# Kernel tuning notes

Hardware: AMD Instinct MI355X
Metric: run time of the kernel (lower is better)

Reference implementation:

```python
import jax, jax.numpy as jnp
import numpy as np

N = 100000   # nodes
E = 3200000  # edges (avg degree 32)
K = 3        # num_stacks
L = 4        # num_layers (ARMA iterations)
H = 16       # hidden channels
C = 1        # num_classes
BN_EPS = 1e-5


def setup_inputs() -> dict:
    key = jax.random.key(0)
    ks = jax.random.split(key, 16)
    s = 0.1  # weight scale
    return {
        "x": jax.random.normal(ks[0], (N, 1), dtype=jnp.float32),
        "edge_index": jax.random.randint(ks[1], (2, E), 0, N, dtype=jnp.int64),
        "edge_attr": jax.random.uniform(ks[2], (E,), dtype=jnp.float32),
        "batch": jnp.zeros((N,), dtype=jnp.int64),
        # ARMAConv 1: 1 -> 16, shared weights
        "w1_init": s * jax.random.normal(ks[3], (K, 1, H), dtype=jnp.float32),
        "w1": s * jax.random.normal(ks[4], (K, H, H), dtype=jnp.float32),
        "w1_root": s * jax.random.normal(ks[5], (K, 1, H), dtype=jnp.float32),
        "b1": s * jax.random.normal(ks[6], (K, 1, H), dtype=jnp.float32),
        "bn1_g": jnp.ones((H,), dtype=jnp.float32),
        "bn1_b": jnp.zeros((H,), dtype=jnp.float32),
        # ARMAConv 2: 16 -> 1, shared weights, act=None
        "w2_init": s * jax.random.normal(ks[7], (K, H, C), dtype=jnp.float32),
        "w2": s * jax.random.normal(ks[8], (K, C, C), dtype=jnp.float32),
        "w2_root": s * jax.random.normal(ks[9], (K, H, C), dtype=jnp.float32),
        "b2": s * jax.random.normal(ks[10], (K, 1, C), dtype=jnp.float32),
    }


def _arma_conv(x, row, col, norm, w_init, w, w_root, b, n_layers, use_relu):
    """PyG ARMAConv with shared_weights=True, eval-mode dropout (identity).
    x: [N,Fin]; returns mean over K stacks: [N,Fout]."""
    n = x.shape[0]
    root = jnp.einsum('nf,kfo->kno', x, w_root)      # [K,N,Fout]
    out = jnp.einsum('nf,kfo->kno', x, w_init)       # [K,N,Fout]
    for t in range(n_layers):
        if t > 0:
            out = jnp.einsum('kno,kop->knp', out, w)
        # message: gather at source, scale by norm; aggregate (scatter-add) at target
        m = (out[:, row, :] * norm[None, :, None]).transpose(1, 0, 2)  # [E,K,F]
        out = jax.ops.segment_sum(m, col, num_segments=n).transpose(1, 0, 2)
        out = out + root + b
        if use_relu:
            out = jax.nn.relu(out)
    return out.mean(axis=0)


def reference(x, edge_index, edge_attr, batch, w1_init, w1, w1_root, b1,
              bn1_g, bn1_b, w2_init, w2, w2_root, b2):
    row, col = edge_index[0], edge_index[1]
    n = x.shape[0]
    # gcn_norm without self-loops: D^{-1/2} A D^{-1/2}
    deg = jax.ops.segment_sum(edge_attr, col, num_segments=n)
    dinv = jnp.where(deg > 0, jax.lax.rsqrt(jnp.maximum(deg, 1e-12)), 0.0)
    norm = dinv[row] * edge_attr * dinv[col]

    h = _arma_conv(x, row, col, norm, w1_init, w1, w1_root, b1, L, True)
    # BatchNorm1d (batch statistics) + ReLU; dropout is identity in eval
    mu = h.mean(axis=0)
    var = h.var(axis=0)
    h = (h - mu) * jax.lax.rsqrt(var + BN_EPS) * bn1_g + bn1_b
    h = jax.nn.relu(h)

    h = _arma_conv(h, row, col, norm, w2_init, w2, w2_root, b2, L, False)
    return jax.nn.sigmoid(h)
```

## Files before the change

### kernel.cpp

```cpp
#include <hip/hip_runtime.h>
#include <math.h>

#define N_NODES 100000
#define N_EDGES 3200000
#define KH 48
#define FDIM 64
#define NH 16
#define BN_EPS 1e-5f
#define NBUCK 196
#define BSHIFT 9
#define BMASK 511
#define EPB 16384
#define NBLK1 196
#define CAP 18432
#define FIX 16777216.0f

typedef unsigned long long u64;
typedef unsigned int u32;
typedef unsigned short u16;

__device__ __forceinline__ u16 f2bf(float f) {
  u32 b = __float_as_uint(f);
  b += 0x7FFFu + ((b >> 16) & 1u);
  return (u16)(b >> 16);
}
__device__ __forceinline__ float bf2f(u32 s) {
  return __uint_as_float(s << 16);
}

__global__ __launch_bounds__(1024) void bucket_scatter_kernel(
    const int* __restrict__ row, const int* __restrict__ col,
    const float* __restrict__ ea, u32* __restrict__ gcur,
    int2* __restrict__ bucketed) {
  __shared__ u32 bins[NBUCK];
  __shared__ u32 base[NBUCK];
  __shared__ u16 rnk[EPB];
  for (int t = threadIdx.x; t < NBUCK; t += 1024) bins[t] = 0;
  __syncthreads();
  int eb = blockIdx.x * EPB;
  for (int it = 0; it < EPB / 1024; ++it) {
    int i = it * 1024 + threadIdx.x;
    int e = eb + i;
    if (e < N_EDGES) rnk[i] = (u16)atomicAdd(&bins[col[e] >> BSHIFT], 1u);
  }
  __syncthreads();
  for (int t = threadIdx.x; t < NBUCK; t += 1024) {
    u32 c = bins[t];
    if (c) base[t] = (u32)t * CAP + atomicAdd(&gcur[t * 8], c);
  }
  __syncthreads();
  for (int it = 0; it < EPB / 1024; ++it) {
    int i = it * 1024 + threadIdx.x;
    int e = eb + i;
    if (e < N_EDGES) {
      int c = col[e];
      int bkt = c >> BSHIFT, cl = c & BMASK;
      u32 pos = base[bkt] + (u32)rnk[i];
      bucketed[pos] = make_int2((cl << 17) | row[e], __float_as_int(ea[e]));
    }
  }
}

__global__ __launch_bounds__(1024) void node_offs_kernel(
    const int2* __restrict__ bucketed, const u32* __restrict__ gcur,
    const float* __restrict__ x,
    int* __restrict__ offs, float* __restrict__ dinv, u16* __restrict__ zx) {
  __shared__ u32 cnt[512];
  __shared__ u32 degf[512];
  __shared__ u32 red[256];
  __shared__ u32 shmeta[2];
  int t = threadIdx.x;
  int b = blockIdx.x;
  if (t < 512) { cnt[t] = 0; degf[t] = 0; }
  if (t < 256) red[t] = (t < b) ? gcur[t * 8] : 0;
  __syncthreads();
  for (int d = 128; d; d >>= 1) {
    if (t < d) red[t] += red[t + d];
    __syncthreads();
  }
  if (t == 0) { shmeta[0] = red[0]; shmeta[1] = gcur[b * 8]; }
  __syncthreads();
  u32 bst = shmeta[0], fill = shmeta[1];
  u32 s_pad = (u32)b * CAP;
  for (u32 i = t; i < fill; i += 1024) {
    int2 v = bucketed[s_pad + i];
    int cl = (v.x >> 17) & BMASK;
    atomicAdd(&cnt[cl], 1u);
    atomicAdd(&degf[cl], (u32)(__int_as_float(v.y) * FIX));
  }
  __syncthreads();
  u32 v0 = (t < 512) ? cnt[t] : 0;
  for (int d = 1; d < 512; d <<= 1) {
    u32 u = (t < 512 && t >= d) ? cnt[t - d] : 0;
    __syncthreads();
    if (t < 512) cnt[t] += u;
    __syncthreads();
  }
  int n = b * 512 + t;
  if (t < 512 && n < N_NODES) {
    offs[n] = (int)(bst + cnt[t] - v0);
    float dg = (float)degf[t] * (1.0f / FIX);
    float dv = dg > 0.f ? rsqrtf(fmaxf(dg, 1e-12f)) : 0.f;
    dinv[n] = dv;
    zx[n] = f2bf(x[n] * dv);
  }
  if (b == 0 && t == 0) offs[N_NODES] = N_EDGES;
}

__global__ __launch_bounds__(1024) void csr_fill_kernel(
    const int2* __restrict__ bucketed, const u32* __restrict__ gcur,
    const int* __restrict__ offs, u32* __restrict__ csr) {
  __shared__ u32 cur[512];
  __shared__ u32 shfill;
  int t = threadIdx.x;
  int b = blockIdx.x;
  int n = b * 512 + t;
  if (t < 512) cur[t] = (n < N_NODES) ? (u32)offs[n] : 0;
  if (t == 0) shfill = gcur[b * 8];
  __syncthreads();
  u32 fill = shfill;
  u32 s_pad = (u32)b * CAP;
  for (u32 i = t; i < fill; i += 1024) {
    int2 v = bucketed[s_pad + i];
    int cl = (v.x >> 17) & BMASK;
    u32 r = (u32)(v.x & 0x1FFFF);
    u16 w = f2bf(__int_as_float(v.y));
    u32 pos = atomicAdd(&cur[cl], 1u);
    csr[pos] = (r << 15) | (u32)w;
  }
}

__global__ __launch_bounds__(256) void sprop_mid_kernel(
    const u32* __restrict__ csr, const int* __restrict__ offs,
    const u16* __restrict__ zx, const float* __restrict__ dinv,
    const float* __restrict__ x,
    const float* __restrict__ w1i, const float* __restrict__ w1r,
    const float* __restrict__ b1, const float* __restrict__ w1,
    u16* __restrict__ tout) {
  int t = blockIdx.x * 256 + threadIdx.x;
  int n = t >> 4, c = t & 15;
  float a = 0.f;
  int s = offs[n], e = offs[n + 1];
  for (int i = s + c; i < e; i += 16) {
    u32 ee = csr[i];
    a += bf2f(ee & 0x7FFFu) * bf2f((u32)zx[ee >> 15]);
  }
#pragma unroll
  for (int o = 8; o; o >>= 1) a += __shfl_xor(a, o, 64);
  float dn = dinv[n];
  float sn = a * dn;
  float xn = x[n];
  int base = (threadIdx.x & 63) & 48;
#pragma unroll
  for (int k = 0; k < 3; ++k) {
    float u = fmaxf(sn * w1i[k * 16 + c] + xn * w1r[k * 16 + c] + b1[k * 16 + c], 0.f);
    float tf = 0.f;
#pragma unroll
    for (int f = 0; f < 16; ++f) tf += __shfl(u, base + f, 64) * w1[k * 256 + f * 16 + c];
    tout[(size_t)n * FDIM + k * 16 + c] = f2bf(tf * dn);
  }
}

__global__ __launch_bounds__(256) void conv1_prop_kernel(
    const u16* __restrict__ tin, u16* __restrict__ tout, float* __restrict__ hbuf,
    const u32* __restrict__ csr, const int* __restrict__ offs,
    const float* __restrict__ dinv, const float* __restrict__ x,
    const float* __restrict__ w1r, const float* __restrict__ b1,
    const float* __restrict__ w1, int do_t) {
  int lane = threadIdx.x & 63;
  int wid = (blockIdx.x * blockDim.x + threadIdx.x) >> 6;
  int nw = (gridDim.x * blockDim.x) >> 6;
  int c = lane;
  bool act = c < KH;
  float rb = act ? w1r[c] : 0.f;
  float bb = act ? b1[c] : 0.f;
  float wreg[16];
  if (do_t) {
    int k = c >> 4, o = c & 15;
    if (act) {
#pragma unroll
      for (int f = 0; f < 16; ++f) wreg[f] = w1[k * 256 + f * 16 + o];
    } else {
#pragma unroll
      for (int f = 0; f < 16; ++f) wreg[f] = 0.f;
    }
  }
  for (int n = wid; n < N_NODES; n += nw) {
    int nu = __builtin_amdgcn_readfirstlane(n);
    int s = offs[nu], e = offs[nu + 1];
    float acc = 0.f;
    int i = s;
    for (; i + 16 <= e; i += 16) {
      u32 e0 = __builtin_nontemporal_load(&csr[i]);
      u32 e1 = __builtin_nontemporal_load(&csr[i + 1]);
      u32 e2 = __builtin_nontemporal_load(&csr[i + 2]);
      u32 e3 = __builtin_nontemporal_load(&csr[i + 3]);
      u32 e4 = __builtin_nontemporal_load(&csr[i + 4]);
      u32 e5 = __builtin_nontemporal_load(&csr[i + 5]);
      u32 e6 = __builtin_nontemporal_load(&csr[i + 6]);
      u32 e7 = __builtin_nontemporal_load(&csr[i + 7]);
      u32 e8 = __builtin_nontemporal_load(&csr[i + 8]);
      u32 e9 = __builtin_nontemporal_load(&csr[i + 9]);
      u32 ea0 = __builtin_nontemporal_load(&csr[i + 10]);
      u32 eb0 = __builtin_nontemporal_load(&csr[i + 11]);
      u32 ec0 = __builtin_nontemporal_load(&csr[i + 12]);
      u32 ed0 = __builtin_nontemporal_load(&csr[i + 13]);
      u32 ee0 = __builtin_nontemporal_load(&csr[i + 14]);
      u32 ef0 = __builtin_nontemporal_load(&csr[i + 15]);
      float v0 = 0.f, v1 = 0.f, v2 = 0.f, v3 = 0.f;
      float v4 = 0.f, v5 = 0.f, v6 = 0.f, v7 = 0.f;
      float v8 = 0.f, v9 = 0.f, va = 0.f, vb = 0.f;
      float vc = 0.f, vd = 0.f, ve = 0.f, vf = 0.f;
      if (act) {
        v0 = bf2f((u32)tin[(e0 >> 15) * FDIM + c]);
        v1 = bf2f((u32)tin[(e1 >> 15) * FDIM + c]);
        v2 = bf2f((u32)tin[(e2 >> 15) * FDIM + c]);
        v3 = bf2f((u32)tin[(e3 >> 15) * FDIM + c]);
        v4 = bf2f((u32)tin[(e4 >> 15) * FDIM + c]);
        v5 = bf2f((u32)tin[(e5 >> 15) * FDIM + c]);
        v6 = bf2f((u32)tin[(e6 >> 15) * FDIM + c]);
        v7 = bf2f((u32)tin[(e7 >> 15) * FDIM + c]);
        v8 = bf2f((u32)tin[(e8 >> 15) * FDIM + c]);
        v9 = bf2f((u32)tin[(e9 >> 15) * FDIM + c]);
        va = bf2f((u32)tin[(ea0 >> 15) * FDIM + c]);
        vb = bf2f((u32)tin[(eb0 >> 15) * FDIM + c]);
        vc = bf2f((u32)tin[(ec0 >> 15) * FDIM + c]);
        vd = bf2f((u32)tin[(ed0 >> 15) * FDIM + c]);
        ve = bf2f((u32)tin[(ee0 >> 15) * FDIM + c]);
        vf = bf2f((u32)tin[(ef0 >> 15) * FDIM + c]);
      }
      acc += bf2f(e0 & 0x7FFFu) * v0 + bf2f(e1 & 0x7FFFu) * v1 +
             bf2f(e2 & 0x7FFFu) * v2 + bf2f(e3 & 0x7FFFu) * v3 +
             bf2f(e4 & 0x7FFFu) * v4 + bf2f(e5 & 0x7FFFu) * v5 +
             bf2f(e6 & 0x7FFFu) * v6 + bf2f(e7 & 0x7FFFu) * v7 +
             bf2f(e8 & 0x7FFFu) * v8 + bf2f(e9 & 0x7FFFu) * v9 +
             bf2f(ea0 & 0x7FFFu) * va + bf2f(eb0 & 0x7FFFu) * vb +
             bf2f(ec0 & 0x7FFFu) * vc + bf2f(ed0 & 0x7FFFu) * vd +
             bf2f(ee0 & 0x7FFFu) * ve + bf2f(ef0 & 0x7FFFu) * vf;
    }
    for (; i + 8 <= e; i += 8) {
      u32 e0 = __builtin_nontemporal_load(&csr[i]);
      u32 e1 = __builtin_nontemporal_load(&csr[i + 1]);
      u32 e2 = __builtin_nontemporal_load(&csr[i + 2]);
      u32 e3 = __builtin_nontemporal_load(&csr[i + 3]);
      u32 e4 = __builtin_nontemporal_load(&csr[i + 4]);
      u32 e5 = __builtin_nontemporal_load(&csr[i + 5]);
      u32 e6 = __builtin_nontemporal_load(&csr[i + 6]);
      u32 e7 = __builtin_nontemporal_load(&csr[i + 7]);
      float v0 = 0.f, v1 = 0.f, v2 = 0.f, v3 = 0.f;
      float v4 = 0.f, v5 = 0.f, v6 = 0.f, v7 = 0.f;
      if (act) {
        v0 = bf2f((u32)tin[(e0 >> 15) * FDIM + c]);
        v1 = bf2f((u32)tin[(e1 >> 15) * FDIM + c]);
        v2 = bf2f((u32)tin[(e2 >> 15) * FDIM + c]);
        v3 = bf2f((u32)tin[(e3 >> 15) * FDIM + c]);
        v4 = bf2f((u32)tin[(e4 >> 15) * FDIM + c]);
        v5 = bf2f((u32)tin[(e5 >> 15) * FDIM + c]);
        v6 = bf2f((u32)tin[(e6 >> 15) * FDIM + c]);
        v7 = bf2f((u32)tin[(e7 >> 15) * FDIM + c]);
      }
      acc += bf2f(e0 & 0x7FFFu) * v0 + bf2f(e1 & 0x7FFFu) * v1 +
             bf2f(e2 & 0x7FFFu) * v2 + bf2f(e3 & 0x7FFFu) * v3 +
             bf2f(e4 & 0x7FFFu) * v4 + bf2f(e5 & 0x7FFFu) * v5 +
             bf2f(e6 & 0x7FFFu) * v6 + bf2f(e7 & 0x7FFFu) * v7;
    }
    for (; i + 4 <= e; i += 4) {
      u32 e0 = __builtin_nontemporal_load(&csr[i]);
      u32 e1 = __builtin_nontemporal_load(&csr[i + 1]);
      u32 e2 = __builtin_nontemporal_load(&csr[i + 2]);
      u32 e3 = __builtin_nontemporal_load(&csr[i + 3]);
      float v0 = 0.f, v1 = 0.f, v2 = 0.f, v3 = 0.f;
      if (act) {
        v0 = bf2f((u32)tin[(e0 >> 15) * FDIM + c]);
        v1 = bf2f((u32)tin[(e1 >> 15) * FDIM + c]);
        v2 = bf2f((u32)tin[(e2 >> 15) * FDIM + c]);
        v3 = bf2f((u32)tin[(e3 >> 15) * FDIM + c]);
      }
      acc += bf2f(e0 & 0x7FFFu) * v0 + bf2f(e1 & 0x7FFFu) * v1 +
             bf2f(e2 & 0x7FFFu) * v2 + bf2f(e3 & 0x7FFFu) * v3;
    }
    for (; i < e; ++i) {
      u32 ee = __builtin_nontemporal_load(&csr[i]);
      if (act) acc += bf2f(ee & 0x7FFFu) * bf2f((u32)tin[(ee >> 15) * FDIM + c]);
    }
    float dn = dinv[nu];
    float u = fmaxf(acc * dn + x[nu] * rb + bb, 0.f);
    if (do_t) {
      float tf = 0.f;
      int base = c & 48;
#pragma unroll
      for (int f = 0; f < 16; ++f) tf += __shfl(u, base + f, 64) * wreg[f];
      if (act) tout[(size_t)nu * FDIM + c] = f2bf(tf * dn);
    } else {
      float m1v = __shfl(u, lane + 16, 64);
      float m2v = __shfl(u, lane + 32, 64);
      if (lane < NH) hbuf[(size_t)nu * NH + lane] = (u + m1v + m2v) * (1.f / 3.f);
    }
  }
}

__global__ __launch_bounds__(256) void bn_stats_kernel(
    const float* __restrict__ h, double* __restrict__ stats) {
  __shared__ float ssum[NH], ssq[NH];
  int tid = threadIdx.x;
  if (tid < NH) { ssum[tid] = 0.f; ssq[tid] = 0.f; }
  __syncthreads();
  int n = blockIdx.x * blockDim.x + tid;
  bool valid = n < N_NODES;
  const float4* p = (const float4*)(h + (size_t)(valid ? n : 0) * NH);
  float hv[NH];
#pragma unroll
  for (int q = 0; q < 4; ++q) {
    float4 v = valid ? p[q] : make_float4(0.f, 0.f, 0.f, 0.f);
    hv[q * 4 + 0] = v.x; hv[q * 4 + 1] = v.y; hv[q * 4 + 2] = v.z; hv[q * 4 + 3] = v.w;
  }
#pragma unroll
  for (int f = 0; f < NH; ++f) {
    float s = hv[f], q = hv[f] * hv[f];
    for (int o = 32; o; o >>= 1) { s += __shfl_xor(s, o, 64); q += __shfl_xor(q, o, 64); }
    if ((tid & 63) == 0) { atomicAdd(&ssum[f], s); atomicAdd(&ssq[f], q); }
  }
  __syncthreads();
  if (tid < NH) {
    atomicAdd(&stats[tid], (double)ssum[tid]);
    atomicAdd(&stats[NH + tid], (double)ssq[tid]);
  }
}

__global__ __launch_bounds__(64) void bn_final_kernel(
    const double* __restrict__ stats, const float* __restrict__ g,
    const float* __restrict__ b, float* __restrict__ sc, float* __restrict__ sh) {
  int f = threadIdx.x;
  if (f < NH) {
    double mu = stats[f] / (double)N_NODES;
    double var = stats[NH + f] / (double)N_NODES - mu * mu;
    float scale = g[f] * (float)(1.0 / sqrt(var + (double)BN_EPS));
    sc[f] = scale;
    sh[f] = b[f] - (float)mu * scale;
  }
}

__global__ __launch_bounds__(256) void conv2_init_kernel(
    const float* __restrict__ h, const float* __restrict__ sc, const float* __restrict__ sh,
    const float* __restrict__ dinv,
    const float* __restrict__ w2i, const float* __restrict__ w2r, const float* __restrict__ b2,
    float* __restrict__ P, float* __restrict__ R) {
  int n = blockIdx.x * blockDim.x + threadIdx.x;
  if (n >= N_NODES) return;
  float u[NH];
#pragma unroll
  for (int f = 0; f < NH; ++f) u[f] = fmaxf(h[(size_t)n * NH + f] * sc[f] + sh[f], 0.f);
  float dn = dinv[n];
#pragma unroll
  for (int k = 0; k < 3; ++k) {
    float r = b2[k], o = 0.f;
#pragma unroll
    for (int f = 0; f < NH; ++f) {
      r += u[f] * w2r[k * NH + f];
      o += u[f] * w2i[k * NH + f];
    }
    R[n * 4 + k] = r;
    P[n * 4 + k] = o * dn;
  }
  R[n * 4 + 3] = 0.f;
  P[n * 4 + 3] = 0.f;
}

__global__ __launch_bounds__(256) void conv2_prop_kernel(
    const float* __restrict__ in4, float* __restrict__ out4, float* __restrict__ y,
    const u32* __restrict__ csr, const int* __restrict__ offs,
    const float* __restrict__ dinv,
    const float* __restrict__ R, const float* __restrict__ w2,
    int scale_w2, int final_out) {
  int t = blockIdx.x * 256 + threadIdx.x;
  int n = t >> 4, sub = t & 15;
  float m0 = 1.f, m1 = 1.f, m2 = 1.f;
  if (scale_w2) { m0 = w2[0]; m1 = w2[1]; m2 = w2[2]; }
  int s = offs[n], e = offs[n + 1];
  float a0 = 0.f, a1 = 0.f, a2 = 0.f;
  for (int i = s + sub; i < e; i += 16) {
    u32 ee = csr[i];
    float w = bf2f(ee & 0x7FFFu);
    const float4 v = *(const float4*)(in4 + (size_t)(ee >> 15) * 4);
    a0 += w * v.x;
    a1 += w * v.y;
    a2 += w * v.z;
  }
#pragma unroll
  for (int o = 8; o; o >>= 1) {
    a0 += __shfl_xor(a0, o, 64);
    a1 += __shfl_xor(a1, o, 64);
    a2 += __shfl_xor(a2, o, 64);
  }
  if (sub == 0) {
    float dn = dinv[n];
    a0 = a0 * dn * m0 + R[n * 4 + 0];
    a1 = a1 * dn * m1 + R[n * 4 + 1];
    a2 = a2 * dn * m2 + R[n * 4 + 2];
    if (final_out) {
      float sm = (a0 + a1 + a2) * (1.f / 3.f);
      y[n] = 1.f / (1.f + expf(-sm));
    } else {
      out4[n * 4 + 0] = a0 * dn;
      out4[n * 4 + 1] = a1 * dn;
      out4[n * 4 + 2] = a2 * dn;
      out4[n * 4 + 3] = 0.f;
    }
  }
}

extern "C" void kernel_launch(void* const* d_in, const int* in_sizes, int n_in,
                              void* d_out, int out_size, void* d_ws, size_t ws_size,
                              hipStream_t stream) {
  const float* x   = (const float*)d_in[0];
  const int*   ei  = (const int*)d_in[1];
  const float* ea  = (const float*)d_in[2];
  const float* w1i = (const float*)d_in[4];
  const float* w1  = (const float*)d_in[5];
  const float* w1r = (const float*)d_in[6];
  const float* b1  = (const float*)d_in[7];
  const float* bng = (const float*)d_in[8];
  const float* bnb = (const float*)d_in[9];
  const float* w2i = (const float*)d_in[10];
  const float* w2  = (const float*)d_in[11];
  const float* w2r = (const float*)d_in[12];
  const float* b2  = (const float*)d_in[13];
  float* y = (float*)d_out;

  const int* row = ei;
  const int* col = ei + N_EDGES;

  char* ws = (char*)d_ws;
  size_t off = 0;
  auto alloc = [&](size_t bytes) -> char* {
    char* p = ws + off;
    off += (bytes + 255) & ~(size_t)255;
    return p;
  };
  u32*    gcur   = (u32*)alloc((size_t)NBUCK * 8 * 4);
  int*    offs   = (int*)alloc((size_t)(N_NODES + 1) * 4);
  float*  dinv   = (float*)alloc((size_t)N_NODES * 4);
  u16*    zx     = (u16*)alloc((size_t)N_NODES * 2);
  double* stats  = (double*)alloc(32 * 8);
  float*  bnsc   = (float*)alloc(16 * 4);
  float*  bnsh   = (float*)alloc(16 * 4);
  int2*   bucketed = (int2*)alloc((size_t)NBUCK * CAP * 8);
  u32*    csr    = (u32*)alloc((size_t)N_EDGES * 4);
  u16*    tA     = (u16*)alloc((size_t)N_NODES * FDIM * 2);
  u16*    tB     = (u16*)alloc((size_t)N_NODES * FDIM * 2);
  float*  hbuf   = (float*)alloc((size_t)N_NODES * NH * 4);
  float*  P2     = (float*)alloc((size_t)N_NODES * 4 * 4);
  float*  Q2     = (float*)alloc((size_t)N_NODES * 4 * 4);
  float*  R2     = (float*)alloc((size_t)N_NODES * 4 * 4);
  (void)ws_size; (void)in_sizes; (void)n_in; (void)out_size;

  hipMemsetAsync(gcur, 0, (size_t)NBUCK * 8 * 4, stream);
  hipMemsetAsync(stats, 0, 32 * 8, stream);

  bucket_scatter_kernel<<<NBLK1, 1024, 0, stream>>>(row, col, ea, gcur, bucketed);
  node_offs_kernel<<<NBUCK, 1024, 0, stream>>>(bucketed, gcur, x, offs, dinv, zx);
  csr_fill_kernel<<<NBUCK, 1024, 0, stream>>>(bucketed, gcur, offs, csr);

  const int NPB = 6250;
  sprop_mid_kernel<<<NPB, 256, 0, stream>>>(csr, offs, zx, dinv, x, w1i, w1r, b1, w1, tA);
  conv1_prop_kernel<<<6250, 256, 0, stream>>>(tA, tB, nullptr, csr, offs, dinv, x, w1r, b1, w1, 1);
  conv1_prop_kernel<<<6250, 256, 0, stream>>>(tB, tA, nullptr, csr, offs, dinv, x, w1r, b1, w1, 1);
  conv1_prop_kernel<<<6250, 256, 0, stream>>>(tA, nullptr, hbuf, csr, offs, dinv, x, w1r, b1, w1, 0);

  bn_stats_kernel<<<(N_NODES + 255) / 256, 256, 0, stream>>>(hbuf, stats);
  bn_final_kernel<<<1, 64, 0, stream>>>(stats, bng, bnb, bnsc, bnsh);
  conv2_init_kernel<<<(N_NODES + 255) / 256, 256, 0, stream>>>(
      hbuf, bnsc, bnsh, dinv, w2i, w2r, b2, P2, R2);

  conv2_prop_kernel<<<NPB, 256, 0, stream>>>(P2, Q2, nullptr, csr, offs, dinv, R2, w2, 0, 0);
  conv2_prop_kernel<<<NPB, 256, 0, stream>>>(Q2, P2, nullptr, csr, offs, dinv, R2, w2, 1, 0);
  conv2_prop_kernel<<<NPB, 256, 0, stream>>>(P2, Q2, nullptr, csr, offs, dinv, R2, w2, 1, 0);
  conv2_prop_kernel<<<NPB, 256, 0, stream>>>(Q2, P2, y, csr, offs, dinv, R2, w2, 1, 1);
}
```

Baseline: 472.2 us.

## Split conv1 propagation per stack with stack-major layout and sub-wave edge parallelism

Stores the conv1 features stack-major (K x N x 16 bf16) instead of interleaved 64-wide rows. Each propagation pass now launches one grid slice per stack. Within a wave, the four 16-lane groups each take a different edge, using vector loads of the CSR plus shuffle reductions, so no lanes sit idle as before. The stack mean moves into the BN stats and conv2 init kernels, which now read three hbuf planes. The trade-off is three times as many CSR reads and more gather requests with narrower 32-byte rows.

```diff
diff --git a/kernel.cpp b/kernel.cpp
--- a/kernel.cpp
+++ b/kernel.cpp
@@ -3,9 +3,8 @@
 
 #define N_NODES 100000
 #define N_EDGES 3200000
-#define KH 48
-#define FDIM 64
 #define NH 16
+#define SST (N_NODES * NH)
 #define BN_EPS 1e-5f
 #define NBUCK 196
 #define BSHIFT 9
@@ -14,10 +13,14 @@
 #define NBLK1 196
 #define CAP 18432
 #define FIX 16777216.0f
+#define NBLKS 6250
+#define NWAVES 25000
 
 typedef unsigned long long u64;
 typedef unsigned int u32;
 typedef unsigned short u16;
+typedef __attribute__((ext_vector_type(4))) unsigned int u32x4;
+typedef __attribute__((ext_vector_type(2))) unsigned int u32x2;
 
 __device__ __forceinline__ u16 f2bf(float f) {
   u32 b = __float_as_uint(f);
@@ -157,144 +160,78 @@
     float tf = 0.f;
 #pragma unroll
     for (int f = 0; f < 16; ++f) tf += __shfl(u, base + f, 64) * w1[k * 256 + f * 16 + c];
-    tout[(size_t)n * FDIM + k * 16 + c] = f2bf(tf * dn);
+    tout[(size_t)k * SST + (size_t)n * NH + c] = f2bf(tf * dn);
   }
 }
 
 __global__ __launch_bounds__(256) void conv1_prop_kernel(
-    const u16* __restrict__ tin, u16* __restrict__ tout, float* __restrict__ hbuf,
+    const u16* __restrict__ tin, u16* __restrict__ tout, float* __restrict__ hbuf3,
     const u32* __restrict__ csr, const int* __restrict__ offs,
     const float* __restrict__ dinv, const float* __restrict__ x,
     const float* __restrict__ w1r, const float* __restrict__ b1,
     const float* __restrict__ w1, int do_t) {
+  int k = blockIdx.x / NBLKS;
+  int bid = blockIdx.x - k * NBLKS;
   int lane = threadIdx.x & 63;
-  int wid = (blockIdx.x * blockDim.x + threadIdx.x) >> 6;
-  int nw = (gridDim.x * blockDim.x) >> 6;
-  int c = lane;
-  bool act = c < KH;
-  float rb = act ? w1r[c] : 0.f;
-  float bb = act ? b1[c] : 0.f;
-  float wreg[16];
+  int sub = lane >> 4;
+  int c = lane & 15;
+  int wid = ((bid << 8) + (int)threadIdx.x) >> 6;
+  const u16* __restrict__ tk = tin + (size_t)k * SST;
+  float rb = w1r[k * NH + c];
+  float bb = b1[k * NH + c];
+  int srcbase = sub * 20;
+  float wreg[4];
   if (do_t) {
-    int k = c >> 4, o = c & 15;
-    if (act) {
-#pragma unroll
-      for (int f = 0; f < 16; ++f) wreg[f] = w1[k * 256 + f * 16 + o];
-    } else {
-#pragma unroll
-      for (int f = 0; f < 16; ++f) wreg[f] = 0.f;
-    }
-  }
-  for (int n = wid; n < N_NODES; n += nw) {
+#pragma unroll
+    for (int j = 0; j < 4; ++j) wreg[j] = w1[k * 256 + (sub * 4 + j) * NH + c];
+  }
+  for (int n = wid; n < N_NODES; n += NWAVES) {
     int nu = __builtin_amdgcn_readfirstlane(n);
     int s = offs[nu], e = offs[nu + 1];
+    float dn = dinv[nu];
+    float xn = x[nu];
     float acc = 0.f;
     int i = s;
+    int la = (4 - (i & 3)) & 3;
+    if (la > e - i) la = e - i;
+    if (sub < la) {
+      u32 ee = __builtin_nontemporal_load(csr + i + sub);
+      acc += bf2f(ee & 0x7FFFu) * bf2f((u32)tk[(ee >> 15) * NH + c]);
+    }
+    i += la;
     for (; i + 16 <= e; i += 16) {
-      u32 e0 = __builtin_nontemporal_load(&csr[i]);
-      u32 e1 = __builtin_nontemporal_load(&csr[i + 1]);
-      u32 e2 = __builtin_nontemporal_load(&csr[i + 2]);
-      u32 e3 = __builtin_nontemporal_load(&csr[i + 3]);
-      u32 e4 = __builtin_nontemporal_load(&csr[i + 4]);
-      u32 e5 = __builtin_nontemporal_load(&csr[i + 5]);
-      u32 e6 = __builtin_nontemporal_load(&csr[i + 6]);
-      u32 e7 = __builtin_nontemporal_load(&csr[i + 7]);
-      u32 e8 = __builtin_nontemporal_load(&csr[i + 8]);
-      u32 e9 = __builtin_nontemporal_load(&csr[i + 9]);
-      u32 ea0 = __builtin_nontemporal_load(&csr[i + 10]);
-      u32 eb0 = __builtin_nontemporal_load(&csr[i + 11]);
-      u32 ec0 = __builtin_nontemporal_load(&csr[i + 12]);
-      u32 ed0 = __builtin_nontemporal_load(&csr[i + 13]);
-      u32 ee0 = __builtin_nontemporal_load(&csr[i + 14]);
-      u32 ef0 = __builtin_nontemporal_load(&csr[i + 15]);
-      float v0 = 0.f, v1 = 0.f, v2 = 0.f, v3 = 0.f;
-      float v4 = 0.f, v5 = 0.f, v6 = 0.f, v7 = 0.f;
-      float v8 = 0.f, v9 = 0.f, va = 0.f, vb = 0.f;
-      float vc = 0.f, vd = 0.f, ve = 0.f, vf = 0.f;
-      if (act) {
-        v0 = bf2f((u32)tin[(e0 >> 15) * FDIM + c]);
-        v1 = bf2f((u32)tin[(e1 >> 15) * FDIM + c]);
-        v2 = bf2f((u32)tin[(e2 >> 15) * FDIM + c]);
-        v3 = bf2f((u32)tin[(e3 >> 15) * FDIM + c]);
-        v4 = bf2f((u32)tin[(e4 >> 15) * FDIM + c]);
-        v5 = bf2f((u32)tin[(e5 >> 15) * FDIM + c]);
-        v6 = bf2f((u32)tin[(e6 >> 15) * FDIM + c]);
-        v7 = bf2f((u32)tin[(e7 >> 15) * FDIM + c]);
-        v8 = bf2f((u32)tin[(e8 >> 15) * FDIM + c]);
-        v9 = bf2f((u32)tin[(e9 >> 15) * FDIM + c]);
-        va = bf2f((u32)tin[(ea0 >> 15) * FDIM + c]);
-        vb = bf2f((u32)tin[(eb0 >> 15) * FDIM + c]);
-        vc = bf2f((u32)tin[(ec0 >> 15) * FDIM + c]);
-        vd = bf2f((u32)tin[(ed0 >> 15) * FDIM + c]);
-        ve = bf2f((u32)tin[(ee0 >> 15) * FDIM + c]);
-        vf = bf2f((u32)tin[(ef0 >> 15) * FDIM + c]);
-      }
-      acc += bf2f(e0 & 0x7FFFu) * v0 + bf2f(e1 & 0x7FFFu) * v1 +
-             bf2f(e2 & 0x7FFFu) * v2 + bf2f(e3 & 0x7FFFu) * v3 +
-             bf2f(e4 & 0x7FFFu) * v4 + bf2f(e5 & 0x7FFFu) * v5 +
-             bf2f(e6 & 0x7FFFu) * v6 + bf2f(e7 & 0x7FFFu) * v7 +
-             bf2f(e8 & 0x7FFFu) * v8 + bf2f(e9 & 0x7FFFu) * v9 +
-             bf2f(ea0 & 0x7FFFu) * va + bf2f(eb0 & 0x7FFFu) * vb +
-             bf2f(ec0 & 0x7FFFu) * vc + bf2f(ed0 & 0x7FFFu) * vd +
-             bf2f(ee0 & 0x7FFFu) * ve + bf2f(ef0 & 0x7FFFu) * vf;
+      u32x4 q = __builtin_nontemporal_load((const u32x4*)(csr + i) + sub);
+      acc += bf2f(q.x & 0x7FFFu) * bf2f((u32)tk[(q.x >> 15) * NH + c]);
+      acc += bf2f(q.y & 0x7FFFu) * bf2f((u32)tk[(q.y >> 15) * NH + c]);
+      acc += bf2f(q.z & 0x7FFFu) * bf2f((u32)tk[(q.z >> 15) * NH + c]);
+      acc += bf2f(q.w & 0x7FFFu) * bf2f((u32)tk[(q.w >> 15) * NH + c]);
     }
     for (; i + 8 <= e; i += 8) {
-      u32 e0 = __builtin_nontemporal_load(&csr[i]);
-      u32 e1 = __builtin_nontemporal_load(&csr[i + 1]);
-      u32 e2 = __builtin_nontemporal_load(&csr[i + 2]);
-      u32 e3 = __builtin_nontemporal_load(&csr[i + 3]);
-      u32 e4 = __builtin_nontemporal_load(&csr[i + 4]);
-      u32 e5 = __builtin_nontemporal_load(&csr[i + 5]);
-      u32 e6 = __builtin_nontemporal_load(&csr[i + 6]);
-      u32 e7 = __builtin_nontemporal_load(&csr[i + 7]);
-      float v0 = 0.f, v1 = 0.f, v2 = 0.f, v3 = 0.f;
-      float v4 = 0.f, v5 = 0.f, v6 = 0.f, v7 = 0.f;
-      if (act) {
-        v0 = bf2f((u32)tin[(e0 >> 15) * FDIM + c]);
-        v1 = bf2f((u32)tin[(e1 >> 15) * FDIM + c]);
-        v2 = bf2f((u32)tin[(e2 >> 15) * FDIM + c]);
-        v3 = bf2f((u32)tin[(e3 >> 15) * FDIM + c]);
-        v4 = bf2f((u32)tin[(e4 >> 15) * FDIM + c]);
-        v5 = bf2f((u32)tin[(e5 >> 15) * FDIM + c]);
-        v6 = bf2f((u32)tin[(e6 >> 15) * FDIM + c]);
-        v7 = bf2f((u32)tin[(e7 >> 15) * FDIM + c]);
-      }
-      acc += bf2f(e0 & 0x7FFFu) * v0 + bf2f(e1 & 0x7FFFu) * v1 +
-             bf2f(e2 & 0x7FFFu) * v2 + bf2f(e3 & 0x7FFFu) * v3 +
-             bf2f(e4 & 0x7FFFu) * v4 + bf2f(e5 & 0x7FFFu) * v5 +
-             bf2f(e6 & 0x7FFFu) * v6 + bf2f(e7 & 0x7FFFu) * v7;
+      u32x2 q = __builtin_nontemporal_load((const u32x2*)(csr + i) + sub);
+      acc += bf2f(q.x & 0x7FFFu) * bf2f((u32)tk[(q.x >> 15) * NH + c]);
+      acc += bf2f(q.y & 0x7FFFu) * bf2f((u32)tk[(q.y >> 15) * NH + c]);
     }
     for (; i + 4 <= e; i += 4) {
-      u32 e0 = __builtin_nontemporal_load(&csr[i]);
-      u32 e1 = __builtin_nontemporal_load(&csr[i + 1]);
-      u32 e2 = __builtin_nontemporal_load(&csr[i + 2]);
-      u32 e3 = __builtin_nontemporal_load(&csr[i + 3]);
-      float v0 = 0.f, v1 = 0.f, v2 = 0.f, v3 = 0.f;
-      if (act) {
-        v0 = bf2f((u32)tin[(e0 >> 15) * FDIM + c]);
-        v1 = bf2f((u32)tin[(e1 >> 15) * FDIM + c]);
-        v2 = bf2f((u32)tin[(e2 >> 15) * FDIM + c]);
-        v3 = bf2f((u32)tin[(e3 >> 15) * FDIM + c]);
-      }
-      acc += bf2f(e0 & 0x7FFFu) * v0 + bf2f(e1 & 0x7FFFu) * v1 +
-             bf2f(e2 & 0x7FFFu) * v2 + bf2f(e3 & 0x7FFFu) * v3;
-    }
-    for (; i < e; ++i) {
-      u32 ee = __builtin_nontemporal_load(&csr[i]);
-      if (act) acc += bf2f(ee & 0x7FFFu) * bf2f((u32)tin[(ee >> 15) * FDIM + c]);
-    }
-    float dn = dinv[nu];
-    float u = fmaxf(acc * dn + x[nu] * rb + bb, 0.f);
+      u32 ee = __builtin_nontemporal_load(csr + i + sub);
+      acc += bf2f(ee & 0x7FFFu) * bf2f((u32)tk[(ee >> 15) * NH + c]);
+    }
+    int rem = e - i;
+    if (sub < rem) {
+      u32 ee = __builtin_nontemporal_load(csr + i + sub);
+      acc += bf2f(ee & 0x7FFFu) * bf2f((u32)tk[(ee >> 15) * NH + c]);
+    }
+    acc += __shfl_xor(acc, 16, 64);
+    acc += __shfl_xor(acc, 32, 64);
+    float u = fmaxf(acc * dn + xn * rb + bb, 0.f);
     if (do_t) {
       float tf = 0.f;
-      int base = c & 48;
-#pragma unroll
-      for (int f = 0; f < 16; ++f) tf += __shfl(u, base + f, 64) * wreg[f];
-      if (act) tout[(size_t)nu * FDIM + c] = f2bf(tf * dn);
+#pragma unroll
+      for (int j = 0; j < 4; ++j) tf += __shfl(u, srcbase + j, 64) * wreg[j];
+      tf += __shfl_xor(tf, 16, 64);
+      tf += __shfl_xor(tf, 32, 64);
+      if (sub == 0) tout[(size_t)k * SST + (size_t)nu * NH + c] = f2bf(tf * dn);
     } else {
-      float m1v = __shfl(u, lane + 16, 64);
-      float m2v = __shfl(u, lane + 32, 64);
-      if (lane < NH) hbuf[(size_t)nu * NH + lane] = (u + m1v + m2v) * (1.f / 3.f);
+      if (sub == 0) hbuf3[(size_t)k * SST + (size_t)nu * NH + c] = u;
     }
   }
 }
@@ -307,12 +244,20 @@
   __syncthreads();
   int n = blockIdx.x * blockDim.x + tid;
   bool valid = n < N_NODES;
-  const float4* p = (const float4*)(h + (size_t)(valid ? n : 0) * NH);
+  size_t base = (size_t)(valid ? n : 0) * NH;
+  const float4* p0 = (const float4*)(h + base);
+  const float4* p1 = (const float4*)(h + (size_t)SST + base);
+  const float4* p2 = (const float4*)(h + 2 * (size_t)SST + base);
   float hv[NH];
 #pragma unroll
   for (int q = 0; q < 4; ++q) {
-    float4 v = valid ? p[q] : make_float4(0.f, 0.f, 0.f, 0.f);
-    hv[q * 4 + 0] = v.x; hv[q * 4 + 1] = v.y; hv[q * 4 + 2] = v.z; hv[q * 4 + 3] = v.w;
+    float4 a = valid ? p0[q] : make_float4(0.f, 0.f, 0.f, 0.f);
+    float4 b = valid ? p1[q] : make_float4(0.f, 0.f, 0.f, 0.f);
+    float4 d = valid ? p2[q] : make_float4(0.f, 0.f, 0.f, 0.f);
+    hv[q * 4 + 0] = (a.x + b.x + d.x) * (1.f / 3.f);
+    hv[q * 4 + 1] = (a.y + b.y + d.y) * (1.f / 3.f);
+    hv[q * 4 + 2] = (a.z + b.z + d.z) * (1.f / 3.f);
+    hv[q * 4 + 3] = (a.w + b.w + d.w) * (1.f / 3.f);
   }
 #pragma unroll
   for (int f = 0; f < NH; ++f) {
@@ -347,9 +292,13 @@
     float* __restrict__ P, float* __restrict__ R) {
   int n = blockIdx.x * blockDim.x + threadIdx.x;
   if (n >= N_NODES) return;
+  size_t base = (size_t)n * NH;
   float u[NH];
 #pragma unroll
-  for (int f = 0; f < NH; ++f) u[f] = fmaxf(h[(size_t)n * NH + f] * sc[f] + sh[f], 0.f);
+  for (int f = 0; f < NH; ++f) {
+    float m = (h[base + f] + h[(size_t)SST + base + f] + h[2 * (size_t)SST + base + f]) * (1.f / 3.f);
+    u[f] = fmaxf(m * sc[f] + sh[f], 0.f);
+  }
   float dn = dinv[n];
 #pragma unroll
   for (int k = 0; k < 3; ++k) {
@@ -446,9 +395,9 @@
   float*  bnsh   = (float*)alloc(16 * 4);
   int2*   bucketed = (int2*)alloc((size_t)NBUCK * CAP * 8);
   u32*    csr    = (u32*)alloc((size_t)N_EDGES * 4);
-  u16*    tA     = (u16*)alloc((size_t)N_NODES * FDIM * 2);
-  u16*    tB     = (u16*)alloc((size_t)N_NODES * FDIM * 2);
-  float*  hbuf   = (float*)alloc((size_t)N_NODES * NH * 4);
+  u16*    tA     = (u16*)alloc((size_t)3 * SST * 2);
+  u16*    tB     = (u16*)alloc((size_t)3 * SST * 2);
+  float*  hbuf   = (float*)alloc((size_t)3 * SST * 4);
   float*  P2     = (float*)alloc((size_t)N_NODES * 4 * 4);
   float*  Q2     = (float*)alloc((size_t)N_NODES * 4 * 4);
   float*  R2     = (float*)alloc((size_t)N_NODES * 4 * 4);
@@ -463,9 +412,9 @@
 
   const int NPB = 6250;
   sprop_mid_kernel<<<NPB, 256, 0, stream>>>(csr, offs, zx, dinv, x, w1i, w1r, b1, w1, tA);
-  conv1_prop_kernel<<<6250, 256, 0, stream>>>(tA, tB, nullptr, csr, offs, dinv, x, w1r, b1, w1, 1);
-  conv1_prop_kernel<<<6250, 256, 0, stream>>>(tB, tA, nullptr, csr, offs, dinv, x, w1r, b1, w1, 1);
-  conv1_prop_kernel<<<6250, 256, 0, stream>>>(tA, nullptr, hbuf, csr, offs, dinv, x, w1r, b1, w1, 0);
+  conv1_prop_kernel<<<3 * NBLKS, 256, 0, stream>>>(tA, tB, nullptr, csr, offs, dinv, x, w1r, b1, w1, 1);
+  conv1_prop_kernel<<<3 * NBLKS, 256, 0, stream>>>(tB, tA, nullptr, csr, offs, dinv, x, w1r, b1, w1, 1);
+  conv1_prop_kernel<<<3 * NBLKS, 256, 0, stream>>>(tA, nullptr, hbuf, csr, offs, dinv, x, w1r, b1, w1, 0);
 
   bn_stats_kernel<<<(N_NODES + 255) / 256, 256, 0, stream>>>(hbuf, stats);
   bn_final_kernel<<<1, 64, 0, stream>>>(stats, bng, bnb, bnsc, bnsh);
```

After: 740.9 us. 1.57x slower.
